# Performance work log

Hardware: AMD Instinct MI355X
Metric: run time of the kernel (lower is better)

## Reference

```python
import jax, jax.numpy as jnp
import numpy as np

B, S, V, D, H, DK, DFF, L = 2, 1024, 513, 512, 8, 64, 2048, 6
PAD_IDX = -1.0
EPS_GPE = 0.1

def _sinusoid_table(n_position, d_hid):
    pos = np.arange(n_position)[:, None].astype(np.float64)
    i = np.arange(d_hid)[None, :]
    angle = pos / np.power(10000.0, 2 * (i // 2) / d_hid)
    tab = np.zeros((n_position, d_hid), dtype=np.float32)
    tab[:, 0::2] = np.sin(angle[:, 0::2])
    tab[:, 1::2] = np.cos(angle[:, 1::2])
    return jnp.asarray(tab)

_POS_TABLE = _sinusoid_table(2048, D)

def _ln(x, g, b, eps=1e-6):
    m = x.mean(-1, keepdims=True)
    v = x.var(-1, keepdims=True)
    return (x - m) * jax.lax.rsqrt(v + eps) * g + b

def _mha(x_q, x_kv, wq_, wk_, wv_, wo_, mask, g, b):
    Bq, Sq, _ = x_q.shape
    Skv = x_kv.shape[1]
    q = (x_q @ wq_).reshape(Bq, Sq, H, DK).transpose(0, 2, 1, 3)
    k = (x_kv @ wk_).reshape(Bq, Skv, H, DK).transpose(0, 2, 1, 3)
    v = (x_kv @ wv_).reshape(Bq, Skv, H, DK).transpose(0, 2, 1, 3)
    scores = jnp.einsum('bhqd,bhkd->bhqk', q, k) / np.float32(np.sqrt(DK))
    scores = jnp.where(mask[:, None], scores, jnp.float32(-1e9))
    attn = jax.nn.softmax(scores, axis=-1)
    out = jnp.einsum('bhqk,bhkd->bhqd', attn, v).transpose(0, 2, 1, 3).reshape(Bq, Sq, D)
    return _ln(x_q + out @ wo_, g, b)

def _forward(dec_in, prev_dec_out, trg, adj, graph_length, gr_mask, gr_pos_enc_kernel,
             emb_w1, emb_b1, emb_w2, emb_b2, emb_w3, emb_b3, ln0_g, ln0_b,
             wq, wk, wv, wo, ln1_g, ln1_b,
             cq, ck, cv, co, ln2_g, ln2_b,
             ffn_w1, ffn_b1, ffn_w2, ffn_b2, ln3_g, ln3_b,
             p_w1, p_b1, p_w2, p_b2, p_w3, p_b3):
    # masks (n_ensemble = 1 so dec_in[:, :, 0, :] == dec_in)
    causal = jnp.tril(jnp.ones((S, S), bool))
    slf_mask = jnp.all(dec_in != PAD_IDX, -1)[:, None, :] & causal          # [B,S,S]
    enc_mask = jnp.all(prev_dec_out != PAD_IDX, -1)[:, None, :]             # [B,1,S]
    # word-embedding MLP: 513 -> 513 -> 513 -> 512
    h = jax.nn.relu(dec_in @ emb_w1 + emb_b1)
    h = jax.nn.relu(h @ emb_w2 + emb_b2)
    h = h @ emb_w3 + emb_b3                                                 # [B,S,D]
    # propagation graph positional encoding (k = 0..2, un-normalized branch)
    w = (1.0 - EPS_GPE) ** jnp.arange(gr_pos_enc_kernel.shape[1], dtype=jnp.float32)
    base = _POS_TABLE[:S]                                                   # [S,D]
    emb = jnp.einsum('k,bkst,td->bsd', w, gr_pos_enc_kernel, base) / w.sum()
    h = _ln(h + emb, ln0_g, ln0_b)
    for i in range(L):
        h = _mha(h, h, wq[i], wk[i], wv[i], wo[i], slf_mask, ln1_g[i], ln1_b[i])
        h = _mha(h, prev_dec_out, cq[i], ck[i], cv[i], co[i], enc_mask, ln2_g[i], ln2_b[i])
        f = jax.nn.relu(h @ ffn_w1[i] + ffn_b1[i]) @ ffn_w2[i] + ffn_b2[i]
        h = _ln(h + f, ln3_g[i], ln3_b[i])
    # projection head: 512 -> 513 -> 513 -> 513
    z = jax.nn.relu(h @ p_w1 + p_b1)
    z = jax.nn.relu(z @ p_w2 + p_b2)
    return z @ p_w3 + p_b3                                                  # [B,S,V]

def setup_inputs():
    key = jax.random.key(0)
    ks = jax.random.split(key, 24)
    def xavier(k, shape):
        lim = np.float32(np.sqrt(6.0 / (shape[-2] + shape[-1])))
        return jax.random.uniform(k, shape, jnp.float32, -lim, lim)
    inp = {}
    inp['dec_in'] = jax.random.uniform(ks[0], (B, S, V), jnp.float32)
    inp['prev_dec_out'] = jax.random.normal(ks[1], (B, S, D), jnp.float32)
    inp['trg'] = jnp.zeros((B, S, V), jnp.float32)
    inp['adj'] = jnp.zeros((B, S, S), jnp.float32)
    inp['graph_length'] = jnp.zeros((B, S, 10), jnp.float32)
    inp['gr_mask'] = jnp.zeros((B, 1, S, S), jnp.float32)
    gk = jax.random.uniform(ks[2], (B, 3, S, S), jnp.float32)
    inp['gr_pos_enc_kernel'] = gk / jnp.sum(gk, -1, keepdims=True)  # row-stochastic diffusion kernels
    SZ = max(V, D)  # sz_intermed = 513
    inp['emb_w1'] = xavier(ks[3], (V, SZ)); inp['emb_b1'] = jnp.zeros((SZ,))
    inp['emb_w2'] = xavier(ks[4], (SZ, SZ)); inp['emb_b2'] = jnp.zeros((SZ,))
    inp['emb_w3'] = xavier(ks[5], (SZ, D)); inp['emb_b3'] = jnp.zeros((D,))
    inp['ln0_g'] = jnp.ones((D,)); inp['ln0_b'] = jnp.zeros((D,))
    for name, ki, shp in [('wq', 6, (L, D, D)), ('wk', 7, (L, D, D)), ('wv', 8, (L, D, D)), ('wo', 9, (L, D, D)),
                          ('cq', 10, (L, D, D)), ('ck', 11, (L, D, D)), ('cv', 12, (L, D, D)), ('co', 13, (L, D, D)),
                          ('ffn_w1', 14, (L, D, DFF)), ('ffn_w2', 15, (L, DFF, D))]:
        inp[name] = xavier(ks[ki], shp)
    inp['ffn_b1'] = jnp.zeros((L, DFF)); inp['ffn_b2'] = jnp.zeros((L, D))
    inp['ln1_g'] = jnp.ones((L, D)); inp['ln1_b'] = jnp.zeros((L, D))
    inp['ln2_g'] = jnp.ones((L, D)); inp['ln2_b'] = jnp.zeros((L, D))
    inp['ln3_g'] = jnp.ones((L, D)); inp['ln3_b'] = jnp.zeros((L, D))
    inp['p_w1'] = xavier(ks[16], (D, V)); inp['p_b1'] = jnp.zeros((V,))
    inp['p_w2'] = xavier(ks[17], (V, V)); inp['p_b2'] = jnp.zeros((V,))
    inp['p_w3'] = xavier(ks[18], (V, V)); inp['p_b3'] = jnp.zeros((V,))
    return inp

def reference(dec_in, prev_dec_out, trg, adj, graph_length, gr_mask, gr_pos_enc_kernel,
              emb_w1, emb_b1, emb_w2, emb_b2, emb_w3, emb_b3, ln0_g, ln0_b,
              wq, wk, wv, wo, ln1_g, ln1_b,
              cq, ck, cv, co, ln2_g, ln2_b,
              ffn_w1, ffn_b1, ffn_w2, ffn_b2, ln3_g, ln3_b,
              p_w1, p_b1, p_w2, p_b2, p_w3, p_b3):
    return _forward(dec_in, prev_dec_out, trg, adj, graph_length, gr_mask, gr_pos_enc_kernel,
                    emb_w1, emb_b1, emb_w2, emb_b2, emb_w3, emb_b3, ln0_g, ln0_b,
                    wq, wk, wv, wo, ln1_g, ln1_b,
                    cq, ck, cv, co, ln2_g, ln2_b,
                    ffn_w1, ffn_b1, ffn_w2, ffn_b2, ln3_g, ln3_b,
                    p_w1, p_b1, p_w2, p_b2, p_w3, p_b3)
```

## Files before the change

### kernel.cpp

```cpp
#include <hip/hip_runtime.h>
#include <hip/hip_bf16.h>
#include <stdint.h>

#define BB 2
#define SS 1024
#define VV 513
#define VP 576
#define DD 512
#define HH 8
#define DKK 64
#define DFFN 2048
#define LL 6
#define MM (BB * SS)

typedef __bf16 bf16x8 __attribute__((ext_vector_type(8)));
typedef float f32x4 __attribute__((ext_vector_type(4)));
typedef unsigned short us8 __attribute__((ext_vector_type(8)));

static __device__ inline unsigned short f2bf(float f) {
  union { float f; unsigned u; } v; v.f = f;
  unsigned u = v.u;
  unsigned r = (u + 0x7FFFu + ((u >> 16) & 1u)) >> 16;
  return (unsigned short)r;
}

static __device__ inline bf16x8 ldfrag(const unsigned short* p) {
  us8 r = *(const us8*)p;
  return __builtin_bit_cast(bf16x8, r);
}

typedef __attribute__((address_space(3))) void lds_void;
typedef const __attribute__((address_space(1))) void glb_void;
static __device__ inline void gl_lds16(const void* g, void* l) {
  __builtin_amdgcn_global_load_lds((glb_void*)g, (lds_void*)l, 16, 0, 0);
}

static __device__ inline bf16x8 ldfrag_swz(const unsigned short* base, int row, int kloc) {
  const unsigned byte = (unsigned)(row * 128 + kloc * 2) ^ (unsigned)((row & 7) << 4);
  return ldfrag((const unsigned short*)((const char*)base + byte));
}

static __device__ inline int rot3(int x) { return (x == 2) ? 0 : x + 1; }

struct GemmP {
  const unsigned short* A;
  const unsigned short* B0; const unsigned short* B1; const unsigned short* B2;
  const float* bias;
  float* C;
  unsigned short* D0; unsigned short* D1; unsigned short* D2;
  int Kp, Np, ldc, Nreal, relu;
};

template<int NB, int NT>
__global__ __launch_bounds__(256)
void gemm_tpl(GemmP p)
{
  constexpr int FN = NT / 32;
  __shared__ unsigned short Al[3][64 * 64];
  __shared__ unsigned short Bl[3][NT * 64];
  const int tid = threadIdx.x;
  const int l = tid & 63, w = tid >> 6;
  const int wm = w >> 1, wn = w & 1;
  const int lr = l & 15, lg = l >> 4;

  const int nbn = p.Np / NT;
  int sel = 0, bx = blockIdx.x;
  if (NB > 1) { sel = bx / nbn; bx -= sel * nbn; }
  const unsigned short* Bmat = p.B0;
  if (NB > 1 && sel == 1) Bmat = p.B1;
  if (NB > 2 && sel == 2) Bmat = p.B2;
  const int m0 = blockIdx.y << 6, n0 = bx * NT;

  f32x4 acc[2][FN];
  const f32x4 zf = {0.f, 0.f, 0.f, 0.f};
#pragma unroll
  for (int i = 0; i < 2; ++i)
#pragma unroll
    for (int j = 0; j < FN; ++j) acc[i][j] = zf;

  const size_t Kp = (size_t)p.Kp;
  const unsigned short* Abase = p.A + (size_t)m0 * Kp;
  const unsigned short* Bbase = Bmat + (size_t)n0 * Kp;

  auto stage = [&](int buf, int kt) {
    const int k0 = kt << 6;
#pragma unroll
    for (int j = 0; j < 2; ++j) {
      const int ti = j * 256 + tid;
      const int row = ti >> 3;
      const int ch = (ti & 7) ^ (row & 7);
      gl_lds16(Abase + (size_t)row * Kp + k0 + ch * 8, &Al[buf][ti * 8]);
    }
#pragma unroll
    for (int j = 0; j < FN; ++j) {
      const int ti = j * 256 + tid;
      const int row = ti >> 3;
      const int ch = (ti & 7) ^ (row & 7);
      gl_lds16(Bbase + (size_t)row * Kp + k0 + ch * 8, &Bl[buf][ti * 8]);
    }
  };

  const int nt = p.Kp >> 6;
  stage(0, 0);
  if (nt > 1) stage(1, 1);
  int cb = 0, sb = 2;

  for (int kt = 0; kt < nt; ++kt) {
    if (kt + 1 < nt) {
      if constexpr (FN == 2) asm volatile("s_waitcnt vmcnt(4)" ::: "memory");
      else                   asm volatile("s_waitcnt vmcnt(6)" ::: "memory");
    } else {
      asm volatile("s_waitcnt vmcnt(0)" ::: "memory");
    }
    __builtin_amdgcn_s_barrier();
    if (kt + 2 < nt) { stage(sb, kt + 2); sb = rot3(sb); }
#pragma unroll
    for (int ks = 0; ks < 2; ++ks) {
      bf16x8 af[2], bfv[FN];
#pragma unroll
      for (int mf = 0; mf < 2; ++mf)
        af[mf] = ldfrag_swz(Al[cb], wm * 32 + mf * 16 + lr, ks * 32 + lg * 8);
#pragma unroll
      for (int nf = 0; nf < FN; ++nf)
        bfv[nf] = ldfrag_swz(Bl[cb], wn * (NT / 2) + nf * 16 + lr, ks * 32 + lg * 8);
#pragma unroll
      for (int mf = 0; mf < 2; ++mf)
#pragma unroll
        for (int nf = 0; nf < FN; ++nf)
          acc[mf][nf] = __builtin_amdgcn_mfma_f32_16x16x32_bf16(af[mf], bfv[nf], acc[mf][nf], 0, 0, 0);
    }
    cb = rot3(cb);
  }

  unsigned short* Dsel = p.D0;
  if (NB > 1 && sel == 1) Dsel = p.D1;
  if (NB > 2 && sel == 2) Dsel = p.D2;
#pragma unroll
  for (int mf = 0; mf < 2; ++mf) {
#pragma unroll
    for (int r = 0; r < 4; ++r) {
      const int grow = m0 + wm * 32 + mf * 16 + (lg << 2) + r;
#pragma unroll
      for (int nf = 0; nf < FN; ++nf) {
        const int gcol = n0 + wn * (NT / 2) + nf * 16 + lr;
        float v = acc[mf][nf][r];
        if (p.bias && gcol < p.Nreal) v += p.bias[gcol];
        if (p.relu) v = fmaxf(v, 0.f);
        if (Dsel) Dsel[(size_t)grow * p.Np + gcol] = f2bf(v);
        if (p.C && gcol < p.Nreal) p.C[(size_t)grow * p.ldc + gcol] = v;
      }
    }
  }
}

struct GemmBat {
  const unsigned short* A;
  const unsigned short* B[12];
  unsigned short* D[12];
  int Kp, Np;
};

__global__ __launch_bounds__(256)
void gemm_bat(GemmBat p)
{
  __shared__ unsigned short Al[3][64 * 64];
  __shared__ unsigned short Bl[3][64 * 64];
  const int tid = threadIdx.x;
  const int l = tid & 63, w = tid >> 6;
  const int wm = w >> 1, wn = w & 1;
  const int lr = l & 15, lg = l >> 4;

  const int nbn = p.Np >> 6;
  const int sel = blockIdx.x / nbn;
  const int bx = blockIdx.x - sel * nbn;
  const unsigned short* Bmat = p.B[sel];
  unsigned short* Dmat = p.D[sel];
  const int m0 = blockIdx.y << 6, n0 = bx << 6;

  f32x4 acc[2][2];
  const f32x4 zf = {0.f, 0.f, 0.f, 0.f};
#pragma unroll
  for (int i = 0; i < 2; ++i)
#pragma unroll
    for (int j = 0; j < 2; ++j) acc[i][j] = zf;

  const size_t Kp = (size_t)p.Kp;
  const unsigned short* Abase = p.A + (size_t)m0 * Kp;
  const unsigned short* Bbase = Bmat + (size_t)n0 * Kp;

  auto stage = [&](int buf, int kt) {
    const int k0 = kt << 6;
#pragma unroll
    for (int j = 0; j < 2; ++j) {
      const int ti = j * 256 + tid;
      const int row = ti >> 3;
      const int ch = (ti & 7) ^ (row & 7);
      gl_lds16(Abase + (size_t)row * Kp + k0 + ch * 8, &Al[buf][ti * 8]);
    }
#pragma unroll
    for (int j = 0; j < 2; ++j) {
      const int ti = j * 256 + tid;
      const int row = ti >> 3;
      const int ch = (ti & 7) ^ (row & 7);
      gl_lds16(Bbase + (size_t)row * Kp + k0 + ch * 8, &Bl[buf][ti * 8]);
    }
  };

  const int nt = p.Kp >> 6;
  stage(0, 0);
  if (nt > 1) stage(1, 1);
  int cb = 0, sb = 2;

  for (int kt = 0; kt < nt; ++kt) {
    if (kt + 1 < nt) asm volatile("s_waitcnt vmcnt(4)" ::: "memory");
    else             asm volatile("s_waitcnt vmcnt(0)" ::: "memory");
    __builtin_amdgcn_s_barrier();
    if (kt + 2 < nt) { stage(sb, kt + 2); sb = rot3(sb); }
#pragma unroll
    for (int ks = 0; ks < 2; ++ks) {
      bf16x8 af[2], bfv[2];
#pragma unroll
      for (int mf = 0; mf < 2; ++mf)
        af[mf] = ldfrag_swz(Al[cb], wm * 32 + mf * 16 + lr, ks * 32 + lg * 8);
#pragma unroll
      for (int nf = 0; nf < 2; ++nf)
        bfv[nf] = ldfrag_swz(Bl[cb], wn * 32 + nf * 16 + lr, ks * 32 + lg * 8);
#pragma unroll
      for (int mf = 0; mf < 2; ++mf)
#pragma unroll
        for (int nf = 0; nf < 2; ++nf)
          acc[mf][nf] = __builtin_amdgcn_mfma_f32_16x16x32_bf16(af[mf], bfv[nf], acc[mf][nf], 0, 0, 0);
    }
    cb = rot3(cb);
  }

#pragma unroll
  for (int mf = 0; mf < 2; ++mf) {
#pragma unroll
    for (int r = 0; r < 4; ++r) {
      const int grow = m0 + wm * 32 + mf * 16 + (lg << 2) + r;
#pragma unroll
      for (int nf = 0; nf < 2; ++nf) {
        const int gcol = n0 + wn * 32 + nf * 16 + lr;
        Dmat[(size_t)grow * p.Np + gcol] = f2bf(acc[mf][nf][r]);
      }
    }
  }
}

__global__ __launch_bounds__(256)
void vtrans_kernel(const unsigned short* __restrict__ src, unsigned short* __restrict__ dst)
{
  __shared__ unsigned short t[64][72];
  const int s0 = blockIdx.x << 6, h = blockIdx.y;
  const int b = blockIdx.z & 1, li = blockIdx.z >> 1;
  const unsigned short* vb = src + (size_t)li * MM * DD;
  unsigned short* vbT = dst + (size_t)li * MM * DD;
  const int tid = threadIdx.x;
  const int rr = tid >> 2, cbase = (tid & 3) * 2;
#pragma unroll
  for (int j = 0; j < 2; ++j) {
    const int ch = cbase + j;
    *(us8*)&t[rr][ch * 8] = *(const us8*)(vb + ((size_t)(b * SS) + s0 + rr) * DD + h * DKK + ch * 8);
  }
  __syncthreads();
#pragma unroll
  for (int j = 0; j < 2; ++j) {
    const int ch = cbase + j;
    us8 o;
#pragma unroll
    for (int e = 0; e < 8; ++e) o[e] = t[ch * 8 + e][rr];
    *(us8*)(vbT + (((size_t)(b * HH) + h) * DKK + rr) * SS + s0 + ch * 8) = o;
  }
}

template<int CAUSAL>
__global__ __launch_bounds__(128)
void attn_kernel(const unsigned short* __restrict__ Qb,
                 const unsigned short* __restrict__ Kb,
                 const unsigned short* __restrict__ VbT,
                 unsigned short* __restrict__ Ob,
                 const float* __restrict__ maskadd)
{
  __shared__ unsigned short Kl[3][64 * 64];
  __shared__ unsigned short Vl[3][64 * 64];
  __shared__ unsigned short Pl[2 * 16 * 72];
  const int tid = threadIdx.x;
  const int l = tid & 63, w = tid >> 6;
  const int qt = blockIdx.x, h = blockIdx.y, b = blockIdx.z;
  const int lr = l & 15, lg = l >> 4;
  const int qbase = qt * 32 + w * 16;

  bf16x8 qf[2];
  {
    const unsigned short* qrow = Qb + ((size_t)(b * SS) + qbase + lr) * DD + h * DKK;
    qf[0] = ldfrag(qrow + (lg << 3));
    qf[1] = ldfrag(qrow + 32 + (lg << 3));
  }

  const unsigned short* Kbase = Kb + (size_t)(b * SS) * DD + h * DKK;
  const unsigned short* Vbase = VbT + ((size_t)(b * HH) + h) * DKK * SS;

  auto stage = [&](int buf, int kt) {
#pragma unroll
    for (int j = 0; j < 4; ++j) {
      const int ti = j * 128 + tid;
      const int row = ti >> 3;
      const int ch = (ti & 7) ^ (row & 7);
      gl_lds16(Kbase + (size_t)(kt * 64 + row) * DD + ch * 8, &Kl[buf][ti * 8]);
    }
#pragma unroll
    for (int j = 0; j < 4; ++j) {
      const int ti = j * 128 + tid;
      const int row = ti >> 3;
      const int ch = (ti & 7) ^ (row & 7);
      gl_lds16(Vbase + (size_t)row * SS + kt * 64 + ch * 8, &Vl[buf][ti * 8]);
    }
  };

  f32x4 accO[4];
  const f32x4 zf = {0.f, 0.f, 0.f, 0.f};
#pragma unroll
  for (int i = 0; i < 4; ++i) accO[i] = zf;
  float mold[4] = {-1e30f, -1e30f, -1e30f, -1e30f};
  float lsum[4] = {0.f, 0.f, 0.f, 0.f};

  const int ktmax = CAUSAL ? ((qt >> 1) + 1) : (SS / 64);
  stage(0, 0);
  if (ktmax > 1) stage(1, 1);
  int cb = 0, sb = 2;

  for (int kt = 0; kt < ktmax; ++kt) {
    if (kt + 1 < ktmax) asm volatile("s_waitcnt vmcnt(8)" ::: "memory");
    else                asm volatile("s_waitcnt vmcnt(0)" ::: "memory");
    __builtin_amdgcn_s_barrier();
    if (kt + 2 < ktmax) { stage(sb, kt + 2); sb = rot3(sb); }
    float sc[4][4];
    __builtin_amdgcn_s_setprio(1);
#pragma unroll
    for (int nf = 0; nf < 4; ++nf) {
      f32x4 s = zf;
      bf16x8 k0 = ldfrag_swz(Kl[cb], nf * 16 + lr, lg * 8);
      bf16x8 k1 = ldfrag_swz(Kl[cb], nf * 16 + lr, 32 + lg * 8);
      s = __builtin_amdgcn_mfma_f32_16x16x32_bf16(qf[0], k0, s, 0, 0, 0);
      s = __builtin_amdgcn_mfma_f32_16x16x32_bf16(qf[1], k1, s, 0, 0, 0);
      const int kglob = kt * 64 + nf * 16 + lr;
      const float madd = maskadd[b * SS + kglob];
#pragma unroll
      for (int r = 0; r < 4; ++r) {
        const int qglob = qbase + (lg << 2) + r;
        sc[nf][r] = (CAUSAL && kglob > qglob) ? -1e9f : s[r] * 0.125f + madd;
      }
    }
    __builtin_amdgcn_s_setprio(0);
#pragma unroll
    for (int r = 0; r < 4; ++r) {
      float mloc = fmaxf(fmaxf(sc[0][r], sc[1][r]), fmaxf(sc[2][r], sc[3][r]));
#pragma unroll
      for (int off = 1; off < 16; off <<= 1)
        mloc = fmaxf(mloc, __shfl_xor(mloc, off, 64));
      const float mnew = fmaxf(mold[r], mloc);
      const float corr = __expf(mold[r] - mnew);
      float ps = 0.f;
#pragma unroll
      for (int nf = 0; nf < 4; ++nf) {
        const float pv = __expf(sc[nf][r] - mnew);
        sc[nf][r] = pv;
        ps += pv;
      }
#pragma unroll
      for (int off = 1; off < 16; off <<= 1)
        ps += __shfl_xor(ps, off, 64);
      lsum[r] = lsum[r] * corr + ps;
#pragma unroll
      for (int nf = 0; nf < 4; ++nf) accO[nf][r] *= corr;
      mold[r] = mnew;
    }
    unsigned short* pw = &Pl[w * 16 * 72];
#pragma unroll
    for (int nf = 0; nf < 4; ++nf)
#pragma unroll
      for (int r = 0; r < 4; ++r)
        pw[((lg << 2) + r) * 72 + nf * 16 + lr] = f2bf(sc[nf][r]);
    bf16x8 pa0 = ldfrag(&pw[lr * 72 + (lg << 3)]);
    bf16x8 pa1 = ldfrag(&pw[lr * 72 + 32 + (lg << 3)]);
    __builtin_amdgcn_s_setprio(1);
#pragma unroll
    for (int nf = 0; nf < 4; ++nf) {
      bf16x8 v0 = ldfrag_swz(Vl[cb], nf * 16 + lr, lg * 8);
      bf16x8 v1 = ldfrag_swz(Vl[cb], nf * 16 + lr, 32 + lg * 8);
      accO[nf] = __builtin_amdgcn_mfma_f32_16x16x32_bf16(pa0, v0, accO[nf], 0, 0, 0);
      accO[nf] = __builtin_amdgcn_mfma_f32_16x16x32_bf16(pa1, v1, accO[nf], 0, 0, 0);
    }
    __builtin_amdgcn_s_setprio(0);
    cb = rot3(cb);
  }
#pragma unroll
  for (int r = 0; r < 4; ++r) {
    const float inv = 1.f / lsum[r];
    const size_t orow = ((size_t)(b * SS) + qbase + (lg << 2) + r) * DD + h * DKK;
#pragma unroll
    for (int nf = 0; nf < 4; ++nf)
      Ob[orow + nf * 16 + lr] = f2bf(accO[nf][r] * inv);
  }
}

__global__ __launch_bounds__(256)
void addln_kernel(const float* __restrict__ a, const float* __restrict__ c,
                  const float* __restrict__ g, const float* __restrict__ bb,
                  float* __restrict__ hf, unsigned short* __restrict__ hb)
{
  const int row = blockIdx.x * 4 + (threadIdx.x >> 6);
  const int l = threadIdx.x & 63;
  const float* ar = a + (size_t)row * DD + l * 8;
  const float* cr = c + (size_t)row * DD + l * 8;
  f32x4 x0 = *(const f32x4*)ar + *(const f32x4*)cr;
  f32x4 x1 = *(const f32x4*)(ar + 4) + *(const f32x4*)(cr + 4);
  float sum = x0[0] + x0[1] + x0[2] + x0[3] + x1[0] + x1[1] + x1[2] + x1[3];
#pragma unroll
  for (int off = 1; off < 64; off <<= 1) sum += __shfl_xor(sum, off, 64);
  const float mean = sum * (1.f / 512.f);
  float vs = 0.f;
#pragma unroll
  for (int j = 0; j < 4; ++j) { float d0 = x0[j] - mean; float d1 = x1[j] - mean; vs += d0 * d0 + d1 * d1; }
#pragma unroll
  for (int off = 1; off < 64; off <<= 1) vs += __shfl_xor(vs, off, 64);
  const float rs = rsqrtf(vs * (1.f / 512.f) + 1e-6f);
  const f32x4 g0 = *(const f32x4*)(g + l * 8), g1 = *(const f32x4*)(g + l * 8 + 4);
  const f32x4 b0 = *(const f32x4*)(bb + l * 8), b1 = *(const f32x4*)(bb + l * 8 + 4);
  f32x4 o0, o1;
  us8 ob;
#pragma unroll
  for (int j = 0; j < 4; ++j) {
    o0[j] = (x0[j] - mean) * rs * g0[j] + b0[j];
    o1[j] = (x1[j] - mean) * rs * g1[j] + b1[j];
    ob[j] = f2bf(o0[j]); ob[j + 4] = f2bf(o1[j]);
  }
  float* of = hf + (size_t)row * DD + l * 8;
  *(f32x4*)of = o0; *(f32x4*)(of + 4) = o1;
  *(us8*)(hb + (size_t)row * DD + l * 8) = ob;
}

__global__ __launch_bounds__(64)
void rowvalid_kernel(const float* __restrict__ x, int n, float* __restrict__ out)
{
  const int row = blockIdx.x, l = threadIdx.x;
  const float* xr = x + (size_t)row * n;
  int ok = 1;
  for (int j = l; j < n; j += 64) ok &= (xr[j] != -1.0f) ? 1 : 0;
  ok = __all(ok) ? 1 : 0;
  if (l == 0) out[row] = ok ? 0.f : -1e9f;
}

__global__ void postable_kernel(unsigned short* __restrict__ tabT)
{
  const int i = blockIdx.x * blockDim.x + threadIdx.x;
  if (i >= DD * SS) return;
  const int d = i >> 10, s = i & 1023;
  const float ex = (float)(2 * (d >> 1)) * (1.0f / (float)DD);
  const float ang = (float)s * exp2f(ex * -13.287712379549449f);
  tabT[i] = f2bf((d & 1) ? cosf(ang) : sinf(ang));
}

__global__ void gpec_kernel(const float* __restrict__ gk, unsigned short* __restrict__ Mb)
{
  const int i = blockIdx.x * blockDim.x + threadIdx.x;
  if (i >= BB * SS * SS) return;
  const int b = i / (SS * SS);
  const int rem = i - b * (SS * SS);
  const float* p = gk + (size_t)b * 3 * SS * SS + rem;
  Mb[i] = f2bf((p[0] + 0.9f * p[SS * SS] + 0.81f * p[2 * SS * SS]) * (1.0f / 2.71f));
}

__global__ __launch_bounds__(256)
void wconv_kernel(const float* __restrict__ W, unsigned short* __restrict__ WT,
                  int K, int N, int Kp, int Np)
{
  __shared__ float t[64][65];
  const float* Wl = W + (size_t)blockIdx.z * K * N;
  unsigned short* WTl = WT + (size_t)blockIdx.z * Np * Kp;
  const int n0 = blockIdx.x << 6, k0 = blockIdx.y << 6;
  const int tid = threadIdx.x;
  const int cx = tid & 63, ry = tid >> 6;
#pragma unroll
  for (int i = 0; i < 16; ++i) {
    const int kk = k0 + ry + i * 4, nn = n0 + cx;
    t[ry + i * 4][cx] = (kk < K && nn < N) ? Wl[(size_t)kk * N + nn] : 0.f;
  }
  __syncthreads();
#pragma unroll
  for (int i = 0; i < 16; ++i) {
    const int nn = n0 + ry + i * 4, kk = k0 + cx;
    WTl[(size_t)nn * Kp + kk] = f2bf(t[cx][ry + i * 4]);
  }
}

struct WconvB { const float* W[8]; unsigned short* WT[8]; };
__global__ __launch_bounds__(256)
void wconv8_kernel(WconvB p)
{
  __shared__ float t[64][65];
  const int z = blockIdx.z;
  const int wi = z / LL, li = z - wi * LL;
  const float* Wl = p.W[wi] + (size_t)li * DD * DD;
  unsigned short* WTl = p.WT[wi] + (size_t)li * DD * DD;
  const int n0 = blockIdx.x << 6, k0 = blockIdx.y << 6;
  const int cx = threadIdx.x & 63, ry = threadIdx.x >> 6;
#pragma unroll
  for (int i = 0; i < 16; ++i)
    t[ry + i * 4][cx] = Wl[(size_t)(k0 + ry + i * 4) * DD + n0 + cx];
  __syncthreads();
#pragma unroll
  for (int i = 0; i < 16; ++i)
    WTl[(size_t)(n0 + ry + i * 4) * DD + k0 + cx] = f2bf(t[cx][ry + i * 4]);
}

__global__ void aconv_kernel(const float* __restrict__ A, unsigned short* __restrict__ Ab,
                             int N, int Np, int total)
{
  const int i = blockIdx.x * blockDim.x + threadIdx.x;
  if (i >= total) return;
  const int row = i / Np, col = i - row * Np;
  Ab[i] = (col < N) ? f2bf(A[(size_t)row * N + col]) : (unsigned short)0;
}

static inline void g1(hipStream_t s, const unsigned short* A, const unsigned short* B,
                      const float* bias, float* C, unsigned short* D,
                      int Kp, int Np, int ldc, int Nreal, int relu)
{
  GemmP p{};
  p.A = A; p.B0 = B; p.bias = bias; p.C = C; p.D0 = D;
  p.Kp = Kp; p.Np = Np; p.ldc = ldc; p.Nreal = Nreal; p.relu = relu;
  gemm_tpl<1, 64><<<dim3(Np >> 6, MM >> 6), 256, 0, s>>>(p);
}

static inline void g1w(hipStream_t s, const unsigned short* A, const unsigned short* B,
                       const float* bias, unsigned short* D, int Kp, int Np, int relu)
{
  GemmP p{};
  p.A = A; p.B0 = B; p.bias = bias; p.D0 = D;
  p.Kp = Kp; p.Np = Np; p.ldc = Np; p.Nreal = Np; p.relu = relu;
  gemm_tpl<1, 128><<<dim3(Np >> 7, MM >> 6), 256, 0, s>>>(p);
}

static inline void g3(hipStream_t s, const unsigned short* A, const unsigned short* B0,
                      const unsigned short* B1, const unsigned short* B2,
                      unsigned short* D0, unsigned short* D1, unsigned short* D2,
                      int Kp, int Np)
{
  GemmP p{};
  p.A = A; p.B0 = B0; p.B1 = B1; p.B2 = B2; p.D0 = D0; p.D1 = D1; p.D2 = D2;
  p.Kp = Kp; p.Np = Np; p.ldc = Np; p.Nreal = Np; p.relu = 0;
  gemm_tpl<3, 64><<<dim3(3 * (Np >> 6), MM >> 6), 256, 0, s>>>(p);
}

extern "C" void kernel_launch(void* const* d_in, const int* in_sizes, int n_in,
                              void* d_out, int out_size, void* d_ws, size_t ws_size,
                              hipStream_t stream)
{
  (void)in_sizes; (void)n_in; (void)out_size; (void)ws_size;
  const float* dec_in = (const float*)d_in[0];
  const float* prev   = (const float*)d_in[1];
  const float* gk     = (const float*)d_in[6];
  const float* emb_w1 = (const float*)d_in[7];
  const float* emb_b1 = (const float*)d_in[8];
  const float* emb_w2 = (const float*)d_in[9];
  const float* emb_b2 = (const float*)d_in[10];
  const float* emb_w3 = (const float*)d_in[11];
  const float* emb_b3 = (const float*)d_in[12];
  const float* ln0_g  = (const float*)d_in[13];
  const float* ln0_b  = (const float*)d_in[14];
  const float* wq     = (const float*)d_in[15];
  const float* wk     = (const float*)d_in[16];
  const float* wv     = (const float*)d_in[17];
  const float* wo     = (const float*)d_in[18];
  const float* cq     = (const float*)d_in[19];
  const float* ck     = (const float*)d_in[20];
  const float* cv     = (const float*)d_in[21];
  const float* co     = (const float*)d_in[22];
  const float* ffn_w1 = (const float*)d_in[23];
  const float* ffn_w2 = (const float*)d_in[24];
  const float* ffn_b1 = (const float*)d_in[25];
  const float* ffn_b2 = (const float*)d_in[26];
  const float* ln1_g  = (const float*)d_in[27];
  const float* ln1_b  = (const float*)d_in[28];
  const float* ln2_g  = (const float*)d_in[29];
  const float* ln2_b  = (const float*)d_in[30];
  const float* ln3_g  = (const float*)d_in[31];
  const float* ln3_b  = (const float*)d_in[32];
  const float* p_w1   = (const float*)d_in[33];
  const float* p_b1   = (const float*)d_in[34];
  const float* p_w2   = (const float*)d_in[35];
  const float* p_b2   = (const float*)d_in[36];
  const float* p_w3   = (const float*)d_in[37];
  const float* p_b3   = (const float*)d_in[38];

  char* wsp = (char*)d_ws;
  auto carve = [&](size_t bytes) { char* r = wsp; wsp += (bytes + 255) & ~(size_t)255; return r; };

  unsigned short* decb  = (unsigned short*)carve((size_t)MM * VP * 2);
  unsigned short* prevb = (unsigned short*)carve((size_t)MM * DD * 2);
  float*          hf    = (float*)carve((size_t)MM * DD * 4);
  unsigned short* hb    = (unsigned short*)carve((size_t)MM * DD * 2);
  float*          xf1   = (float*)carve((size_t)MM * DD * 4);
  unsigned short* tb1   = (unsigned short*)carve((size_t)MM * DFFN * 2);
  unsigned short* Mbb   = tb1;
  float*          xf2   = (float*)((char*)tb1 + (size_t)MM * SS * 2);
  unsigned short* tb2a  = (unsigned short*)carve((size_t)MM * VP * 2);
  unsigned short* tb2b  = (unsigned short*)carve((size_t)MM * VP * 2);
  unsigned short* qb    = (unsigned short*)carve((size_t)MM * DD * 2);
  unsigned short* kb    = (unsigned short*)carve((size_t)MM * DD * 2);
  unsigned short* vb    = (unsigned short*)carve((size_t)MM * DD * 2);
  unsigned short* vbT   = (unsigned short*)carve((size_t)MM * DD * 2);
  float* kvs = (float*)carve((size_t)MM * 4);
  float* kve = (float*)carve((size_t)MM * 4);
  unsigned short* postabt = (unsigned short*)carve((size_t)DD * SS * 2);
  unsigned short* ew1t  = (unsigned short*)carve((size_t)VP * VP * 2);
  unsigned short* ew2t  = (unsigned short*)carve((size_t)VP * VP * 2);
  unsigned short* ew3t  = (unsigned short*)carve((size_t)DD * VP * 2);
  unsigned short* wqt   = (unsigned short*)carve((size_t)LL * DD * DD * 2);
  unsigned short* wkt   = (unsigned short*)carve((size_t)LL * DD * DD * 2);
  unsigned short* wvt   = (unsigned short*)carve((size_t)LL * DD * DD * 2);
  unsigned short* wot   = (unsigned short*)carve((size_t)LL * DD * DD * 2);
  unsigned short* cqt   = (unsigned short*)carve((size_t)LL * DD * DD * 2);
  unsigned short* ckt   = (unsigned short*)carve((size_t)LL * DD * DD * 2);
  unsigned short* cvt   = (unsigned short*)carve((size_t)LL * DD * DD * 2);
  unsigned short* cot   = (unsigned short*)carve((size_t)LL * DD * DD * 2);
  unsigned short* f1t   = (unsigned short*)carve((size_t)LL * DFFN * DD * 2);
  unsigned short* f2t   = (unsigned short*)carve((size_t)LL * DD * DFFN * 2);
  unsigned short* p1t   = (unsigned short*)carve((size_t)VP * DD * 2);
  unsigned short* p2t   = (unsigned short*)carve((size_t)VP * VP * 2);
  unsigned short* p3t   = (unsigned short*)carve((size_t)VP * VP * 2);
  unsigned short* ckall = (unsigned short*)carve((size_t)LL * MM * DD * 2);
  unsigned short* cvall = (unsigned short*)carve((size_t)LL * MM * DD * 2);
  unsigned short* cvbT  = (unsigned short*)carve((size_t)LL * MM * DD * 2);

  const dim3 agrid(SS / 32, HH, BB);

  rowvalid_kernel<<<MM, 64, 0, stream>>>(dec_in, VV, kvs);
  rowvalid_kernel<<<MM, 64, 0, stream>>>(prev, DD, kve);
  aconv_kernel<<<(MM * VP + 255) / 256, 256, 0, stream>>>(dec_in, decb, VV, VP, MM * VP);
  aconv_kernel<<<(MM * DD + 255) / 256, 256, 0, stream>>>(prev, prevb, DD, DD, MM * DD);
  postable_kernel<<<(DD * SS + 255) / 256, 256, 0, stream>>>(postabt);
  gpec_kernel<<<(BB * SS * SS + 255) / 256, 256, 0, stream>>>(gk, Mbb);

  {
    WconvB wb{};
    wb.W[0] = wq; wb.W[1] = wk; wb.W[2] = wv; wb.W[3] = wo;
    wb.W[4] = cq; wb.W[5] = ck; wb.W[6] = cv; wb.W[7] = co;
    wb.WT[0] = wqt; wb.WT[1] = wkt; wb.WT[2] = wvt; wb.WT[3] = wot;
    wb.WT[4] = cqt; wb.WT[5] = ckt; wb.WT[6] = cvt; wb.WT[7] = cot;
    wconv8_kernel<<<dim3(8, 8, 8 * LL), 256, 0, stream>>>(wb);
  }
  wconv_kernel<<<dim3(9, 9, 1), 256, 0, stream>>>(emb_w1, ew1t, VV, VV, VP, VP);
  wconv_kernel<<<dim3(9, 9, 1), 256, 0, stream>>>(emb_w2, ew2t, VV, VV, VP, VP);
  wconv_kernel<<<dim3(8, 9, 1), 256, 0, stream>>>(emb_w3, ew3t, VV, DD, VP, DD);
  wconv_kernel<<<dim3(32, 8, LL), 256, 0, stream>>>(ffn_w1, f1t, DD, DFFN, DD, DFFN);
  wconv_kernel<<<dim3(8, 32, LL), 256, 0, stream>>>(ffn_w2, f2t, DFFN, DD, DFFN, DD);
  wconv_kernel<<<dim3(9, 8, 1), 256, 0, stream>>>(p_w1, p1t, DD, VV, DD, VP);
  wconv_kernel<<<dim3(9, 9, 1), 256, 0, stream>>>(p_w2, p2t, VV, VV, VP, VP);
  wconv_kernel<<<dim3(9, 9, 1), 256, 0, stream>>>(p_w3, p3t, VV, VV, VP, VP);

  {
    GemmBat p{};
    p.A = prevb; p.Kp = DD; p.Np = DD;
    for (int i = 0; i < LL; ++i) {
      p.B[2 * i]     = ckt + (size_t)i * DD * DD;
      p.B[2 * i + 1] = cvt + (size_t)i * DD * DD;
      p.D[2 * i]     = ckall + (size_t)i * MM * DD;
      p.D[2 * i + 1] = cvall + (size_t)i * MM * DD;
    }
    gemm_bat<<<dim3(12 * (DD >> 6), MM >> 6), 256, 0, stream>>>(p);
    vtrans_kernel<<<dim3(16, 8, 2 * LL), 256, 0, stream>>>(cvall, cvbT);
  }

  g1(stream, decb, ew1t, emb_b1, nullptr, tb2a, VP, VP, VP, VV, 1);
  g1(stream, tb2a, ew2t, emb_b2, nullptr, tb2b, VP, VP, VP, VV, 1);
  g1(stream, tb2b, ew3t, emb_b3, xf1, nullptr, VP, DD, DD, DD, 0);
  g1(stream, Mbb, postabt, nullptr, xf2, nullptr, SS, DD, DD, DD, 0);
  addln_kernel<<<MM / 4, 256, 0, stream>>>(xf1, xf2, ln0_g, ln0_b, hf, hb);

  for (int i = 0; i < LL; ++i) {
    const size_t od = (size_t)i * DD * DD;
    g3(stream, hb, wqt + od, wkt + od, wvt + od, qb, kb, vb, DD, DD);
    vtrans_kernel<<<dim3(16, 8, 2), 256, 0, stream>>>(vb, vbT);
    attn_kernel<1><<<agrid, 128, 0, stream>>>(qb, kb, vbT, qb, kvs);
    g1(stream, qb, wot + od, nullptr, xf1, nullptr, DD, DD, DD, DD, 0);
    addln_kernel<<<MM / 4, 256, 0, stream>>>(hf, xf1, ln1_g + i * DD, ln1_b + i * DD, hf, hb);
    g1(stream, hb, cqt + od, nullptr, nullptr, qb, DD, DD, DD, DD, 0);
    attn_kernel<0><<<agrid, 128, 0, stream>>>(qb, ckall + (size_t)i * MM * DD,
                                              cvbT + (size_t)i * MM * DD, qb, kve);
    g1(stream, qb, cot + od, nullptr, xf1, nullptr, DD, DD, DD, DD, 0);
    addln_kernel<<<MM / 4, 256, 0, stream>>>(hf, xf1, ln2_g + i * DD, ln2_b + i * DD, hf, hb);
    g1w(stream, hb, f1t + (size_t)i * DFFN * DD, ffn_b1 + i * DFFN, tb1, DD, DFFN, 1);
    g1(stream, tb1, f2t + (size_t)i * DD * DFFN, ffn_b2 + i * DD, xf1, nullptr, DFFN, DD, DD, DD, 0);
    addln_kernel<<<MM / 4, 256, 0, stream>>>(hf, xf1, ln3_g + i * DD, ln3_b + i * DD, hf, hb);
  }

  g1(stream, hb, p1t, p_b1, nullptr, tb2a, DD, VP, VP, VV, 1);
  g1(stream, tb2a, p2t, p_b2, nullptr, tb2b, VP, VP, VP, VV, 1);
  g1(stream, tb2b, p3t, p_b3, (float*)d_out, nullptr, VP, VP, VV, VV, 0);
}
```

Baseline: 1.172 ms.

## Fuse residual LayerNorm into GEMMs and write V transposed from projection epilogues

Replaces the separate add+LayerNorm kernels with a GEMM variant in which the last-arriving block per 64-row stripe, chosen via an atomic counter, performs the residual add and LayerNorm. The QKV and cross-KV projection epilogues now write V directly in the transposed per-head layout, removing the vtrans kernels. Row-validity and bf16 conversion of the inputs are merged into one prep kernel. This cuts kernel launches and intermediate traffic, at the cost of a serialized LayerNorm tail in one block per stripe, strided 8-byte stores for V, and a per-call counter memset.

Result: slower. 1.875 ms (+60.0%).

```diff
diff --git a/kernel.cpp b/kernel.cpp
--- a/kernel.cpp
+++ b/kernel.cpp
@@ -16,6 +16,7 @@
 typedef __bf16 bf16x8 __attribute__((ext_vector_type(8)));
 typedef float f32x4 __attribute__((ext_vector_type(4)));
 typedef unsigned short us8 __attribute__((ext_vector_type(8)));
+typedef unsigned short us4 __attribute__((ext_vector_type(4)));
 
 static __device__ inline unsigned short f2bf(float f) {
   union { float f; unsigned u; } v; v.f = f;
@@ -51,7 +52,7 @@
   int Kp, Np, ldc, Nreal, relu;
 };
 
-template<int NB, int NT>
+template<int NB, int NT, int TRV>
 __global__ __launch_bounds__(256)
 void gemm_tpl(GemmP p)
 {
@@ -135,6 +136,25 @@
   unsigned short* Dsel = p.D0;
   if (NB > 1 && sel == 1) Dsel = p.D1;
   if (NB > 2 && sel == 2) Dsel = p.D2;
+
+  if (TRV && sel == 2) {
+#pragma unroll
+    for (int mf = 0; mf < 2; ++mf) {
+      const int growb = m0 + wm * 32 + mf * 16 + (lg << 2);
+      const int b = growb >> 10, s = growb & 1023;
+#pragma unroll
+      for (int nf = 0; nf < FN; ++nf) {
+        const int gcol = n0 + wn * (NT / 2) + nf * 16 + lr;
+        const int h = gcol >> 6, d = gcol & 63;
+        us4 t;
+#pragma unroll
+        for (int r = 0; r < 4; ++r) t[r] = f2bf(acc[mf][nf][r]);
+        *(us4*)(Dsel + (((size_t)(b * HH) + h) * DKK + d) * SS + s) = t;
+      }
+    }
+    return;
+  }
+
 #pragma unroll
   for (int mf = 0; mf < 2; ++mf) {
 #pragma unroll
@@ -234,6 +254,24 @@
     cb = rot3(cb);
   }
 
+  if (sel & 1) {
+#pragma unroll
+    for (int mf = 0; mf < 2; ++mf) {
+      const int growb = m0 + wm * 32 + mf * 16 + (lg << 2);
+      const int b = growb >> 10, s = growb & 1023;
+#pragma unroll
+      for (int nf = 0; nf < 2; ++nf) {
+        const int gcol = n0 + wn * 32 + nf * 16 + lr;
+        const int h = gcol >> 6, d = gcol & 63;
+        us4 t;
+#pragma unroll
+        for (int r = 0; r < 4; ++r) t[r] = f2bf(acc[mf][nf][r]);
+        *(us4*)(Dmat + (((size_t)(b * HH) + h) * DKK + d) * SS + s) = t;
+      }
+    }
+    return;
+  }
+
 #pragma unroll
   for (int mf = 0; mf < 2; ++mf) {
 #pragma unroll
@@ -248,29 +286,137 @@
   }
 }
 
+struct GemmLnP {
+  const unsigned short* A;
+  const unsigned short* B;
+  const float* bias;
+  const float* resid;
+  float* tmp;
+  const float* gamma; const float* beta;
+  float* hfout; unsigned short* hbout;
+  int* cnt;
+  int Kp;
+};
+
 __global__ __launch_bounds__(256)
-void vtrans_kernel(const unsigned short* __restrict__ src, unsigned short* __restrict__ dst)
-{
-  __shared__ unsigned short t[64][72];
-  const int s0 = blockIdx.x << 6, h = blockIdx.y;
-  const int b = blockIdx.z & 1, li = blockIdx.z >> 1;
-  const unsigned short* vb = src + (size_t)li * MM * DD;
-  unsigned short* vbT = dst + (size_t)li * MM * DD;
+void gemm_ln(GemmLnP p)
+{
+  __shared__ unsigned short Al[3][64 * 64];
+  __shared__ unsigned short Bl[3][64 * 64];
+  __shared__ int lastflag;
   const int tid = threadIdx.x;
-  const int rr = tid >> 2, cbase = (tid & 3) * 2;
-#pragma unroll
-  for (int j = 0; j < 2; ++j) {
-    const int ch = cbase + j;
-    *(us8*)&t[rr][ch * 8] = *(const us8*)(vb + ((size_t)(b * SS) + s0 + rr) * DD + h * DKK + ch * 8);
-  }
+  const int l = tid & 63, w = tid >> 6;
+  const int wm = w >> 1, wn = w & 1;
+  const int lr = l & 15, lg = l >> 4;
+  const int m0 = blockIdx.y << 6, n0 = blockIdx.x << 6;
+
+  f32x4 acc[2][2];
+  const f32x4 zf = {0.f, 0.f, 0.f, 0.f};
+#pragma unroll
+  for (int i = 0; i < 2; ++i)
+#pragma unroll
+    for (int j = 0; j < 2; ++j) acc[i][j] = zf;
+
+  const size_t Kp = (size_t)p.Kp;
+  const unsigned short* Abase = p.A + (size_t)m0 * Kp;
+  const unsigned short* Bbase = p.B + (size_t)n0 * Kp;
+
+  auto stage = [&](int buf, int kt) {
+    const int k0 = kt << 6;
+#pragma unroll
+    for (int j = 0; j < 2; ++j) {
+      const int ti = j * 256 + tid;
+      const int row = ti >> 3;
+      const int ch = (ti & 7) ^ (row & 7);
+      gl_lds16(Abase + (size_t)row * Kp + k0 + ch * 8, &Al[buf][ti * 8]);
+    }
+#pragma unroll
+    for (int j = 0; j < 2; ++j) {
+      const int ti = j * 256 + tid;
+      const int row = ti >> 3;
+      const int ch = (ti & 7) ^ (row & 7);
+      gl_lds16(Bbase + (size_t)row * Kp + k0 + ch * 8, &Bl[buf][ti * 8]);
+    }
+  };
+
+  const int nt = p.Kp >> 6;
+  stage(0, 0);
+  if (nt > 1) stage(1, 1);
+  int cb = 0, sb = 2;
+
+  for (int kt = 0; kt < nt; ++kt) {
+    if (kt + 1 < nt) asm volatile("s_waitcnt vmcnt(4)" ::: "memory");
+    else             asm volatile("s_waitcnt vmcnt(0)" ::: "memory");
+    __builtin_amdgcn_s_barrier();
+    if (kt + 2 < nt) { stage(sb, kt + 2); sb = rot3(sb); }
+#pragma unroll
+    for (int ks = 0; ks < 2; ++ks) {
+      bf16x8 af[2], bfv[2];
+#pragma unroll
+      for (int mf = 0; mf < 2; ++mf)
+        af[mf] = ldfrag_swz(Al[cb], wm * 32 + mf * 16 + lr, ks * 32 + lg * 8);
+#pragma unroll
+      for (int nf = 0; nf < 2; ++nf)
+        bfv[nf] = ldfrag_swz(Bl[cb], wn * 32 + nf * 16 + lr, ks * 32 + lg * 8);
+#pragma unroll
+      for (int mf = 0; mf < 2; ++mf)
+#pragma unroll
+        for (int nf = 0; nf < 2; ++nf)
+          acc[mf][nf] = __builtin_amdgcn_mfma_f32_16x16x32_bf16(af[mf], bfv[nf], acc[mf][nf], 0, 0, 0);
+    }
+    cb = rot3(cb);
+  }
+
+#pragma unroll
+  for (int mf = 0; mf < 2; ++mf) {
+#pragma unroll
+    for (int r = 0; r < 4; ++r) {
+      const int grow = m0 + wm * 32 + mf * 16 + (lg << 2) + r;
+#pragma unroll
+      for (int nf = 0; nf < 2; ++nf) {
+        const int gcol = n0 + wn * 32 + nf * 16 + lr;
+        float v = acc[mf][nf][r];
+        if (p.bias) v += p.bias[gcol];
+        p.tmp[(size_t)grow * DD + gcol] = v;
+      }
+    }
+  }
+  __threadfence();
+  if (tid == 0) lastflag = (atomicAdd(p.cnt + blockIdx.y, 1) == 7);
   __syncthreads();
-#pragma unroll
-  for (int j = 0; j < 2; ++j) {
-    const int ch = cbase + j;
-    us8 o;
-#pragma unroll
-    for (int e = 0; e < 8; ++e) o[e] = t[ch * 8 + e][rr];
-    *(us8*)(vbT + (((size_t)(b * HH) + h) * DKK + rr) * SS + s0 + ch * 8) = o;
+  if (!lastflag) return;
+  __threadfence();
+
+#pragma unroll 1
+  for (int it = 0; it < 16; ++it) {
+    const int row = m0 + it * 4 + w;
+    const float* ar = p.resid + (size_t)row * DD + l * 8;
+    const float* cr = p.tmp + (size_t)row * DD + l * 8;
+    f32x4 x0 = *(const f32x4*)ar + *(const f32x4*)cr;
+    f32x4 x1 = *(const f32x4*)(ar + 4) + *(const f32x4*)(cr + 4);
+    float sum = x0[0] + x0[1] + x0[2] + x0[3] + x1[0] + x1[1] + x1[2] + x1[3];
+#pragma unroll
+    for (int off = 1; off < 64; off <<= 1) sum += __shfl_xor(sum, off, 64);
+    const float mean = sum * (1.f / 512.f);
+    float vs = 0.f;
+#pragma unroll
+    for (int j = 0; j < 4; ++j) { float d0 = x0[j] - mean, d1 = x1[j] - mean; vs += d0 * d0 + d1 * d1; }
+#pragma unroll
+    for (int off = 1; off < 64; off <<= 1) vs += __shfl_xor(vs, off, 64);
+    const float rs = rsqrtf(vs * (1.f / 512.f) + 1e-6f);
+    const f32x4 g0 = *(const f32x4*)(p.gamma + l * 8), g1 = *(const f32x4*)(p.gamma + l * 8 + 4);
+    const f32x4 b0 = *(const f32x4*)(p.beta + l * 8), b1 = *(const f32x4*)(p.beta + l * 8 + 4);
+    f32x4 o0, o1;
+    us8 ob;
+#pragma unroll
+    for (int j = 0; j < 4; ++j) {
+      o0[j] = (x0[j] - mean) * rs * g0[j] + b0[j];
+      o1[j] = (x1[j] - mean) * rs * g1[j] + b1[j];
+      ob[j] = f2bf(o0[j]); ob[j + 4] = f2bf(o1[j]);
+    }
+    float* of = p.hfout + (size_t)row * DD + l * 8;
+    *(f32x4*)of = o0; *(f32x4*)(of + 4) = o1;
+    *(us8*)(p.hbout + (size_t)row * DD + l * 8) = ob;
   }
 }
 
@@ -405,51 +551,26 @@
   }
 }
 
-__global__ __launch_bounds__(256)
-void addln_kernel(const float* __restrict__ a, const float* __restrict__ c,
-                  const float* __restrict__ g, const float* __restrict__ bb,
-                  float* __restrict__ hf, unsigned short* __restrict__ hb)
-{
-  const int row = blockIdx.x * 4 + (threadIdx.x >> 6);
-  const int l = threadIdx.x & 63;
-  const float* ar = a + (size_t)row * DD + l * 8;
-  const float* cr = c + (size_t)row * DD + l * 8;
-  f32x4 x0 = *(const f32x4*)ar + *(const f32x4*)cr;
-  f32x4 x1 = *(const f32x4*)(ar + 4) + *(const f32x4*)(cr + 4);
-  float sum = x0[0] + x0[1] + x0[2] + x0[3] + x1[0] + x1[1] + x1[2] + x1[3];
-#pragma unroll
-  for (int off = 1; off < 64; off <<= 1) sum += __shfl_xor(sum, off, 64);
-  const float mean = sum * (1.f / 512.f);
-  float vs = 0.f;
-#pragma unroll
-  for (int j = 0; j < 4; ++j) { float d0 = x0[j] - mean; float d1 = x1[j] - mean; vs += d0 * d0 + d1 * d1; }
-#pragma unroll
-  for (int off = 1; off < 64; off <<= 1) vs += __shfl_xor(vs, off, 64);
-  const float rs = rsqrtf(vs * (1.f / 512.f) + 1e-6f);
-  const f32x4 g0 = *(const f32x4*)(g + l * 8), g1 = *(const f32x4*)(g + l * 8 + 4);
-  const f32x4 b0 = *(const f32x4*)(bb + l * 8), b1 = *(const f32x4*)(bb + l * 8 + 4);
-  f32x4 o0, o1;
-  us8 ob;
-#pragma unroll
-  for (int j = 0; j < 4; ++j) {
-    o0[j] = (x0[j] - mean) * rs * g0[j] + b0[j];
-    o1[j] = (x1[j] - mean) * rs * g1[j] + b1[j];
-    ob[j] = f2bf(o0[j]); ob[j + 4] = f2bf(o1[j]);
-  }
-  float* of = hf + (size_t)row * DD + l * 8;
-  *(f32x4*)of = o0; *(f32x4*)(of + 4) = o1;
-  *(us8*)(hb + (size_t)row * DD + l * 8) = ob;
-}
-
+template<int NCOLS, int NPAD>
 __global__ __launch_bounds__(64)
-void rowvalid_kernel(const float* __restrict__ x, int n, float* __restrict__ out)
+void prep_row(const float* __restrict__ x, unsigned short* __restrict__ xb,
+              float* __restrict__ mask)
 {
   const int row = blockIdx.x, l = threadIdx.x;
-  const float* xr = x + (size_t)row * n;
+  const float* xr = x + (size_t)row * NCOLS;
+  unsigned short* ob = xb + (size_t)row * NPAD;
   int ok = 1;
-  for (int j = l; j < n; j += 64) ok &= (xr[j] != -1.0f) ? 1 : 0;
+  for (int j = l; j < NPAD; j += 64) {
+    if (j < NCOLS) {
+      const float v = xr[j];
+      ok &= (v != -1.0f) ? 1 : 0;
+      ob[j] = f2bf(v);
+    } else {
+      ob[j] = 0;
+    }
+  }
   ok = __all(ok) ? 1 : 0;
-  if (l == 0) out[row] = ok ? 0.f : -1e9f;
+  if (l == 0) mask[row] = ok ? 0.f : -1e9f;
 }
 
 __global__ void postable_kernel(unsigned short* __restrict__ tabT)
@@ -515,15 +636,6 @@
     WTl[(size_t)(n0 + ry + i * 4) * DD + k0 + cx] = f2bf(t[cx][ry + i * 4]);
 }
 
-__global__ void aconv_kernel(const float* __restrict__ A, unsigned short* __restrict__ Ab,
-                             int N, int Np, int total)
-{
-  const int i = blockIdx.x * blockDim.x + threadIdx.x;
-  if (i >= total) return;
-  const int row = i / Np, col = i - row * Np;
-  Ab[i] = (col < N) ? f2bf(A[(size_t)row * N + col]) : (unsigned short)0;
-}
-
 static inline void g1(hipStream_t s, const unsigned short* A, const unsigned short* B,
                       const float* bias, float* C, unsigned short* D,
                       int Kp, int Np, int ldc, int Nreal, int relu)
@@ -531,7 +643,7 @@
   GemmP p{};
   p.A = A; p.B0 = B; p.bias = bias; p.C = C; p.D0 = D;
   p.Kp = Kp; p.Np = Np; p.ldc = ldc; p.Nreal = Nreal; p.relu = relu;
-  gemm_tpl<1, 64><<<dim3(Np >> 6, MM >> 6), 256, 0, s>>>(p);
+  gemm_tpl<1, 64, 0><<<dim3(Np >> 6, MM >> 6), 256, 0, s>>>(p);
 }
 
 static inline void g1w(hipStream_t s, const unsigned short* A, const unsigned short* B,
@@ -540,18 +652,17 @@
   GemmP p{};
   p.A = A; p.B0 = B; p.bias = bias; p.D0 = D;
   p.Kp = Kp; p.Np = Np; p.ldc = Np; p.Nreal = Np; p.relu = relu;
-  gemm_tpl<1, 128><<<dim3(Np >> 7, MM >> 6), 256, 0, s>>>(p);
-}
-
-static inline void g3(hipStream_t s, const unsigned short* A, const unsigned short* B0,
-                      const unsigned short* B1, const unsigned short* B2,
-                      unsigned short* D0, unsigned short* D1, unsigned short* D2,
-                      int Kp, int Np)
+  gemm_tpl<1, 128, 0><<<dim3(Np >> 7, MM >> 6), 256, 0, s>>>(p);
+}
+
+static inline void g3t(hipStream_t s, const unsigned short* A, const unsigned short* B0,
+                       const unsigned short* B1, const unsigned short* B2,
+                       unsigned short* D0, unsigned short* D1, unsigned short* D2T)
 {
   GemmP p{};
-  p.A = A; p.B0 = B0; p.B1 = B1; p.B2 = B2; p.D0 = D0; p.D1 = D1; p.D2 = D2;
-  p.Kp = Kp; p.Np = Np; p.ldc = Np; p.Nreal = Np; p.relu = 0;
-  gemm_tpl<3, 64><<<dim3(3 * (Np >> 6), MM >> 6), 256, 0, s>>>(p);
+  p.A = A; p.B0 = B0; p.B1 = B1; p.B2 = B2; p.D0 = D0; p.D1 = D1; p.D2 = D2T;
+  p.Kp = DD; p.Np = DD; p.ldc = DD; p.Nreal = DD; p.relu = 0;
+  gemm_tpl<3, 64, 1><<<dim3(3 * (DD >> 6), MM >> 6), 256, 0, s>>>(p);
 }
 
 extern "C" void kernel_launch(void* const* d_in, const int* in_sizes, int n_in,
@@ -610,7 +721,6 @@
   unsigned short* tb2b  = (unsigned short*)carve((size_t)MM * VP * 2);
   unsigned short* qb    = (unsigned short*)carve((size_t)MM * DD * 2);
   unsigned short* kb    = (unsigned short*)carve((size_t)MM * DD * 2);
-  unsigned short* vb    = (unsigned short*)carve((size_t)MM * DD * 2);
   unsigned short* vbT   = (unsigned short*)carve((size_t)MM * DD * 2);
   float* kvs = (float*)carve((size_t)MM * 4);
   float* kve = (float*)carve((size_t)MM * 4);
@@ -632,15 +742,25 @@
   unsigned short* p2t   = (unsigned short*)carve((size_t)VP * VP * 2);
   unsigned short* p3t   = (unsigned short*)carve((size_t)VP * VP * 2);
   unsigned short* ckall = (unsigned short*)carve((size_t)LL * MM * DD * 2);
-  unsigned short* cvall = (unsigned short*)carve((size_t)LL * MM * DD * 2);
   unsigned short* cvbT  = (unsigned short*)carve((size_t)LL * MM * DD * 2);
+  int* cnts = (int*)carve(19 * 32 * sizeof(int));
 
   const dim3 agrid(SS / 32, HH, BB);
 
-  rowvalid_kernel<<<MM, 64, 0, stream>>>(dec_in, VV, kvs);
-  rowvalid_kernel<<<MM, 64, 0, stream>>>(prev, DD, kve);
-  aconv_kernel<<<(MM * VP + 255) / 256, 256, 0, stream>>>(dec_in, decb, VV, VP, MM * VP);
-  aconv_kernel<<<(MM * DD + 255) / 256, 256, 0, stream>>>(prev, prevb, DD, DD, MM * DD);
+  hipMemsetAsync(cnts, 0, 19 * 32 * sizeof(int), stream);
+  int cslot = 0;
+  auto gln = [&](const unsigned short* A, const unsigned short* B, const float* bias,
+                 const float* resid, float* tmp, const float* gamma, const float* beta,
+                 int Kp) {
+    GemmLnP p{};
+    p.A = A; p.B = B; p.bias = bias; p.resid = resid; p.tmp = tmp;
+    p.gamma = gamma; p.beta = beta; p.hfout = hf; p.hbout = hb;
+    p.cnt = cnts + (cslot++) * 32; p.Kp = Kp;
+    gemm_ln<<<dim3(8, 32), 256, 0, stream>>>(p);
+  };
+
+  prep_row<VV, VP><<<MM, 64, 0, stream>>>(dec_in, decb, kvs);
+  prep_row<DD, DD><<<MM, 64, 0, stream>>>(prev, prevb, kve);
   postable_kernel<<<(DD * SS + 255) / 256, 256, 0, stream>>>(postabt);
   gpec_kernel<<<(BB * SS * SS + 255) / 256, 256, 0, stream>>>(gk, Mbb);
 
@@ -668,33 +788,28 @@
       p.B[2 * i]     = ckt + (size_t)i * DD * DD;
       p.B[2 * i + 1] = cvt + (size_t)i * DD * DD;
       p.D[2 * i]     = ckall + (size_t)i * MM * DD;
-      p.D[2 * i + 1] = cvall + (size_t)i * MM * DD;
+      p.D[2 * i + 1] = cvbT + (size_t)i * MM * DD;
     }
     gemm_bat<<<dim3(12 * (DD >> 6), MM >> 6), 256, 0, stream>>>(p);
-    vtrans_kernel<<<dim3(16, 8, 2 * LL), 256, 0, stream>>>(cvall, cvbT);
   }
 
   g1(stream, decb, ew1t, emb_b1, nullptr, tb2a, VP, VP, VP, VV, 1);
   g1(stream, tb2a, ew2t, emb_b2, nullptr, tb2b, VP, VP, VP, VV, 1);
   g1(stream, tb2b, ew3t, emb_b3, xf1, nullptr, VP, DD, DD, DD, 0);
-  g1(stream, Mbb, postabt, nullptr, xf2, nullptr, SS, DD, DD, DD, 0);
-  addln_kernel<<<MM / 4, 256, 0, stream>>>(xf1, xf2, ln0_g, ln0_b, hf, hb);
+  gln(Mbb, postabt, nullptr, xf1, xf2, ln0_g, ln0_b, SS);
 
   for (int i = 0; i < LL; ++i) {
     const size_t od = (size_t)i * DD * DD;
-    g3(stream, hb, wqt + od, wkt + od, wvt + od, qb, kb, vb, DD, DD);
-    vtrans_kernel<<<dim3(16, 8, 2), 256, 0, stream>>>(vb, vbT);
+    g3t(stream, hb, wqt + od, wkt + od, wvt + od, qb, kb, vbT);
     attn_kernel<1><<<agrid, 128, 0, stream>>>(qb, kb, vbT, qb, kvs);
-    g1(stream, qb, wot + od, nullptr, xf1, nullptr, DD, DD, DD, DD, 0);
-    addln_kernel<<<MM / 4, 256, 0, stream>>>(hf, xf1, ln1_g + i * DD, ln1_b + i * DD, hf, hb);
+    gln(qb, wot + od, nullptr, hf, xf1, ln1_g + i * DD, ln1_b + i * DD, DD);
     g1(stream, hb, cqt + od, nullptr, nullptr, qb, DD, DD, DD, DD, 0);
     attn_kernel<0><<<agrid, 128, 0, stream>>>(qb, ckall + (size_t)i * MM * DD,
                                               cvbT + (size_t)i * MM * DD, qb, kve);
-    g1(stream, qb, cot + od, nullptr, xf1, nullptr, DD, DD, DD, DD, 0);
-    addln_kernel<<<MM / 4, 256, 0, stream>>>(hf, xf1, ln2_g + i * DD, ln2_b + i * DD, hf, hb);
+    gln(qb, cot + od, nullptr, hf, xf1, ln2_g + i * DD, ln2_b + i * DD, DD);
     g1w(stream, hb, f1t + (size_t)i * DFFN * DD, ffn_b1 + i * DFFN, tb1, DD, DFFN, 1);
-    g1(stream, tb1, f2t + (size_t)i * DD * DFFN, ffn_b2 + i * DD, xf1, nullptr, DFFN, DD, DD, DD, 0);
-    addln_kernel<<<MM / 4, 256, 0, stream>>>(hf, xf1, ln3_g + i * DD, ln3_b + i * DD, hf, hb);
+    gln(tb1, f2t + (size_t)i * DD * DFFN, ffn_b2 + i * DD, hf, xf1,
+        ln3_g + i * DD, ln3_b + i * DD, DFFN);
   }
 
   g1(stream, hb, p1t, p_b1, nullptr, tb2a, DD, VP, VP, VV, 1);
```
